# Kernel tuning notes

Hardware: AMD Instinct MI355X
Metric: run time of the kernel (lower is better)

The kernel has to match this reference:

```python
import jax, jax.numpy as jnp
import numpy as np


def setup_inputs() -> dict:
    key = jax.random.key(0)
    pcd = jax.random.normal(key, (8, 4096, 3), dtype=jnp.float32)
    return {"pcd": pcd, "k": 5}


def reference(pcd, k):
    # pcd: [B, N, 3]. Faithful port of MC3DAD_ONNX.get_geometry_features.
    sq = jnp.sum(pcd * pcd, axis=-1)                       # [B, N]
    d2 = sq[:, :, None] + sq[:, None, :] - 2.0 * jnp.einsum('bnd,bmd->bnm', pcd, pcd)
    dist = jnp.sqrt(jnp.maximum(d2, 0.0))                  # [B, N, N], == torch.cdist
    # k nearest neighbors (smallest distances) -> indices only
    _, idx = jax.lax.top_k(-dist, k)                       # idx: [B, N, K]
    # gather neighbor coordinates: [B, N, K, 3]
    neighbors = jax.vmap(lambda p, i: p[i])(pcd, idx)
    centroid = jnp.mean(neighbors, axis=2, keepdims=True)  # [B, N, 1, 3]
    centered = neighbors - centroid                        # [B, N, K, 3]
    # per-point 3x3 covariance: centered^T @ centered / (K-1)
    cov = jnp.einsum('bnkc,bnkd->bncd', centered, centered) / (k - 1)
    trace = jnp.trace(cov, axis1=-2, axis2=-1)             # [B, N]
    curvature = trace / (jnp.sum(trace, axis=-1, keepdims=True) + 1e-8)
    return curvature
```

## Files before the change

kernel.cpp:

```cpp
#include <hip/hip_runtime.h>
#include <hip/hip_bf16.h>


typedef unsigned long long ull;

constexpr int N_PTS  = 4096;
constexpr int BATCH  = 8;
constexpr int KNN    = 5;
constexpr int SEG    = 8;
constexpr int SEGLEN = N_PTS / SEG;
constexpr int QPW    = 8;
constexpr int NTHR   = 1024;
constexpr int QPB    = (NTHR / 64) * QPW;
constexpr int KSLOT  = 16;
constexpr int TRIG   = KSLOT - 4;

__device__ __forceinline__ int swz(int j) { return j + (j >> 9); }

__device__ __forceinline__ ull umin64(ull a, ull b) { return a < b ? a : b; }
__device__ __forceinline__ ull umax64(ull a, ull b) { return a < b ? b : a; }

__device__ __forceinline__ void push5(float dd, int idx,
                                      float d[KNN], int ix[KNN])
{
    float ad = dd; int ai = idx;
    #pragma unroll
    for (int p = 0; p < KNN - 1; ++p) {
        const bool lt = ad < d[p];
        const float md = lt ? ad : d[p];
        const int   mi = lt ? ai : ix[p];
        const float xd = lt ? d[p] : ad;
        const int   xi = lt ? ix[p] : ai;
        d[p] = md; ix[p] = mi; ad = xd; ai = xi;
    }
    const bool lt = ad < d[KNN - 1];
    d[KNN - 1]  = lt ? ad : d[KNN - 1];
    ix[KNN - 1] = lt ? ai : ix[KNN - 1];
}

__device__ __forceinline__ void merge5(ull a[KNN], const ull b[KNN])
{
    const ull r0 = umin64(a[0], b[0]);
    const ull r1 = umin64(umin64(a[1], b[1]), umax64(a[0], b[0]));
    const ull r2 = umin64(umin64(a[2], b[2]),
                          umin64(umax64(a[1], b[0]), umax64(a[0], b[1])));
    const ull r3 = umin64(umin64(a[3], b[3]),
                   umin64(umax64(a[2], b[0]),
                   umin64(umax64(a[1], b[1]), umax64(a[0], b[2]))));
    const ull r4 = umin64(umin64(a[4], b[4]),
                   umin64(umin64(umax64(a[3], b[0]), umax64(a[2], b[1])),
                          umin64(umax64(a[1], b[2]), umax64(a[0], b[3]))));
    a[0] = r0; a[1] = r1; a[2] = r2; a[3] = r3; a[4] = r4;
}

struct KnnShared {
    float4 pts[N_PTS + SEG];
    int    buf[KSLOT * NTHR];
};

__device__ __forceinline__ void drain_buf(int& cnt, const float4 qp,
                                          float dq[KNN], int iq[KNN],
                                          float& tau_q,
                                          const float4* __restrict__ pts,
                                          const int* __restrict__ lanebuf)
{
    for (int j = 0; ; ++j) {
        if (!__any(j < cnt)) break;
        if (j < cnt) {
            const int idx = lanebuf[j * NTHR];
            const float4 c = pts[swz(idx)];
            const float dot = __fadd_rn(__fadd_rn(__fmul_rn(qp.x, c.x),
                                                  __fmul_rn(qp.y, c.y)),
                                        __fmul_rn(qp.z, c.z));
            const float dd = __fsub_rn(__fadd_rn(qp.w, c.w),
                                       __fmul_rn(2.0f, dot));
            push5(dd, idx, dq, iq);
        }
    }
    cnt = 0;
    tau_q = __fsub_rn(dq[KNN - 1], qp.w) + 6e-5f;
}

__global__ __launch_bounds__(NTHR, 4)
void knn_trace_kernel(const float* __restrict__ pcd, float* __restrict__ trace_out)
{
    __shared__ KnnShared sh;

    const int b = blockIdx.y;
    const int t = threadIdx.x;
    const float* __restrict__ batch = pcd + (size_t)b * N_PTS * 3;

    #pragma unroll
    for (int i = 0; i < N_PTS / NTHR; ++i) {
        const int p = t + i * NTHR;
        const float x = batch[p * 3 + 0];
        const float y = batch[p * 3 + 1];
        const float z = batch[p * 3 + 2];
        const float sq = __fadd_rn(__fadd_rn(__fmul_rn(x, x), __fmul_rn(y, y)),
                                   __fmul_rn(z, z));
        sh.pts[swz(p)] = make_float4(x, y, z, sq);
    }
    __syncthreads();

    const int lane = t & 63;
    const int wave = t >> 6;
    const int q    = lane & 7;
    const int s    = lane >> 3;
    const int qbase = blockIdx.x * QPB + wave * QPW;
    const float4 qp = sh.pts[swz(qbase + q)];

    float dq[KNN];
    int   iq[KNN];
    #pragma unroll
    for (int r = 0; r < KNN; ++r) { dq[r] = __builtin_inff(); iq[r] = 0x7fffffff; }

    const float4* __restrict__ seg = sh.pts + (s * SEGLEN + s);
    int* __restrict__ lanebuf = sh.buf + t;

    int   cnt   = 0;
    float tau_q = __builtin_inff();
    const int idx0 = s * SEGLEN;

    for (int m0 = 0; m0 < SEGLEN; m0 += 4) {
        #pragma unroll
        for (int u = 0; u < 4; ++u) {
            const float4 c = seg[m0 + u];
            const float t2 = fmaf(-2.0f,
                                  fmaf(qp.x, c.x,
                                       fmaf(qp.y, c.y, qp.z * c.z)),
                                  c.w);
            const bool keep = t2 < tau_q;
            lanebuf[cnt * NTHR] = idx0 + m0 + u;
            cnt += keep ? 1 : 0;
        }
        if (__any(cnt > TRIG))
            drain_buf(cnt, qp, dq, iq, tau_q, sh.pts, lanebuf);
    }
    drain_buf(cnt, qp, dq, iq, tau_q, sh.pts, lanebuf);

    ull key[KNN];
    #pragma unroll
    for (int r = 0; r < KNN; ++r) {
        const float dist = __fsqrt_rn(fmaxf(dq[r], 0.0f));
        key[r] = ((ull)__float_as_uint(dist) << 32) | (unsigned)iq[r];
    }
    #pragma unroll
    for (int i = 0; i < KNN - 1; ++i)
        #pragma unroll
        for (int p = 0; p < KNN - 1 - i; ++p) {
            const ull lo = umin64(key[p], key[p + 1]);
            const ull hi = umax64(key[p], key[p + 1]);
            key[p] = lo; key[p + 1] = hi;
        }

    #pragma unroll
    for (int mask = 8; mask < 64; mask <<= 1) {
        ull o[KNN];
        #pragma unroll
        for (int r = 0; r < KNN; ++r) o[r] = __shfl_xor(key[r], mask);
        merge5(key, o);
    }

    if (lane < 8) {
        float nx[KNN], ny[KNN], nz[KNN];
        #pragma unroll
        for (int r = 0; r < KNN; ++r) {
            const int sel = (int)(key[r] & 0xffffffffull);
            const float4 p = sh.pts[swz(sel)];
            nx[r] = p.x; ny[r] = p.y; nz[r] = p.z;
        }

        float sx = nx[0], sy = ny[0], sz = nz[0];
        #pragma unroll
        for (int r = 1; r < KNN; ++r) {
            sx = __fadd_rn(sx, nx[r]);
            sy = __fadd_rn(sy, ny[r]);
            sz = __fadd_rn(sz, nz[r]);
        }
        const float cx = __fdiv_rn(sx, 5.0f);
        const float cy = __fdiv_rn(sy, 5.0f);
        const float cz = __fdiv_rn(sz, 5.0f);

        float sxx = 0.0f, syy = 0.0f, szz = 0.0f;
        #pragma unroll
        for (int r = 0; r < KNN; ++r) {
            const float dx = __fsub_rn(nx[r], cx);
            const float dy = __fsub_rn(ny[r], cy);
            const float dz = __fsub_rn(nz[r], cz);
            sxx = __fadd_rn(sxx, __fmul_rn(dx, dx));
            syy = __fadd_rn(syy, __fmul_rn(dy, dy));
            szz = __fadd_rn(szz, __fmul_rn(dz, dz));
        }
        const float trace = __fadd_rn(__fadd_rn(__fmul_rn(sxx, 0.25f),
                                                __fmul_rn(syy, 0.25f)),
                                      __fmul_rn(szz, 0.25f));
        trace_out[(size_t)b * N_PTS + qbase + lane] = trace;
    }
}

__global__ __launch_bounds__(256)
void curvature_kernel(const float* __restrict__ trace, float* __restrict__ out)
{
    __shared__ float red[256];
    const int b = blockIdx.x >> 3;
    const int c = blockIdx.x & 7;
    const int t = threadIdx.x;
    const float* __restrict__ tr = trace + (size_t)b * N_PTS;

    float s = 0.0f;
    #pragma unroll
    for (int i = 0; i < N_PTS / 256; ++i)
        s += tr[t + i * 256];
    red[t] = s;
    __syncthreads();
    #pragma unroll
    for (int o = 128; o > 0; o >>= 1) {
        if (t < o) red[t] += red[t + o];
        __syncthreads();
    }
    const float denom = red[0] + 1e-8f;

    float* __restrict__ ob = out + (size_t)b * N_PTS;
    const int x = c * 512 + t;
    ob[x]       = tr[x]       / denom;
    ob[x + 256] = tr[x + 256] / denom;
}

extern "C" void kernel_launch(void* const* d_in, const int* in_sizes, int n_in,
                              void* d_out, int out_size, void* d_ws, size_t ws_size,
                              hipStream_t stream)
{
    (void)in_sizes; (void)n_in; (void)out_size; (void)ws_size;
    const float* pcd = (const float*)d_in[0];
    float* trace = (float*)d_ws;
    float* out = (float*)d_out;

    dim3 gridA(N_PTS / QPB, BATCH);
    knn_trace_kernel<<<gridA, NTHR, 0, stream>>>(pcd, trace);
    curvature_kernel<<<BATCH * 8, 256, 0, stream>>>(trace, out);
}
```

Measured before the change: 135.8 us.

## Replace LDS candidate buffer with bitmask scan and wave-shared pruning threshold

The per-lane LDS index buffer is replaced by register bitmasks: each chunk is scanned to build a keep-mask, and the mask is then drained with ctz. Each lane now handles two queries, reusing every loaded candidate point, and blocks drop to 512 threads. After each chunk the running 5th-best distance is min-reduced across the 8 segment lanes of a query and used as a shared pruning threshold. Chunk sizes grow from 8 to 32 so pruning can start early. This removes LDS buffer traffic and tightens pruning, at the cost of more shuffles and per-chunk synchronisation points.

```diff
diff --git a/kernel.cpp b/kernel.cpp
--- a/kernel.cpp
+++ b/kernel.cpp
@@ -1,5 +1,4 @@
 #include <hip/hip_runtime.h>
-#include <hip/hip_bf16.h>
 
 
 typedef unsigned long long ull;
@@ -9,11 +8,9 @@
 constexpr int KNN    = 5;
 constexpr int SEG    = 8;
 constexpr int SEGLEN = N_PTS / SEG;
-constexpr int QPW    = 8;
-constexpr int NTHR   = 1024;
+constexpr int NTHR   = 512;
+constexpr int QPW    = 16;
 constexpr int QPB    = (NTHR / 64) * QPW;
-constexpr int KSLOT  = 16;
-constexpr int TRIG   = KSLOT - 4;
 
 __device__ __forceinline__ int swz(int j) { return j + (j >> 9); }
 
@@ -53,38 +50,89 @@
     a[0] = r0; a[1] = r1; a[2] = r2; a[3] = r3; a[4] = r4;
 }
 
-struct KnnShared {
-    float4 pts[N_PTS + SEG];
-    int    buf[KSLOT * NTHR];
-};
-
-__device__ __forceinline__ void drain_buf(int& cnt, const float4 qp,
-                                          float dq[KNN], int iq[KNN],
-                                          float& tau_q,
-                                          const float4* __restrict__ pts,
-                                          const int* __restrict__ lanebuf)
-{
-    for (int j = 0; ; ++j) {
-        if (!__any(j < cnt)) break;
-        if (j < cnt) {
-            const int idx = lanebuf[j * NTHR];
+__device__ __forceinline__ void sort5(ull key[KNN])
+{
+    #pragma unroll
+    for (int i = 0; i < KNN - 1; ++i)
+        #pragma unroll
+        for (int p = 0; p < KNN - 1 - i; ++p) {
+            const ull lo = umin64(key[p], key[p + 1]);
+            const ull hi = umax64(key[p], key[p + 1]);
+            key[p] = lo; key[p + 1] = hi;
+        }
+}
+
+template<int CSZ>
+__device__ __forceinline__ void scan_chunk(const float4* __restrict__ seg, int step0,
+                                           const float4 p0, const float4 p1,
+                                           const float tau0, const float tau1,
+                                           unsigned& m0, unsigned& m1)
+{
+    unsigned a = 0, b = 0;
+    #pragma unroll 8
+    for (int u = 0; u < CSZ; ++u) {
+        const float4 c = seg[step0 + u];
+        const float f0 = fmaf(-2.0f, fmaf(p0.x, c.x,
+                                          fmaf(p0.y, c.y, p0.z * c.z)), c.w);
+        const float f1 = fmaf(-2.0f, fmaf(p1.x, c.x,
+                                          fmaf(p1.y, c.y, p1.z * c.z)), c.w);
+        a = (a << 1) | (f0 < tau0 ? 1u : 0u);
+        b = (b << 1) | (f1 < tau1 ? 1u : 0u);
+    }
+    m0 = a; m1 = b;
+}
+
+__device__ __forceinline__ void drain_pair(unsigned r0, unsigned r1, int base,
+                                           const float4 p0, const float4 p1,
+                                           float* __restrict__ d0, int* __restrict__ i0,
+                                           float* __restrict__ d1, int* __restrict__ i1,
+                                           const float4* __restrict__ pts)
+{
+    while (__any((r0 | r1) != 0)) {
+        if (r0) {
+            const int bpos = __builtin_ctz(r0);
+            r0 &= r0 - 1;
+            const int idx = base + bpos;
             const float4 c = pts[swz(idx)];
-            const float dot = __fadd_rn(__fadd_rn(__fmul_rn(qp.x, c.x),
-                                                  __fmul_rn(qp.y, c.y)),
-                                        __fmul_rn(qp.z, c.z));
-            const float dd = __fsub_rn(__fadd_rn(qp.w, c.w),
+            const float dot = __fadd_rn(__fadd_rn(__fmul_rn(p0.x, c.x),
+                                                  __fmul_rn(p0.y, c.y)),
+                                        __fmul_rn(p0.z, c.z));
+            const float dd = __fsub_rn(__fadd_rn(p0.w, c.w),
                                        __fmul_rn(2.0f, dot));
-            push5(dd, idx, dq, iq);
-        }
-    }
-    cnt = 0;
-    tau_q = __fsub_rn(dq[KNN - 1], qp.w) + 6e-5f;
-}
-
-__global__ __launch_bounds__(NTHR, 4)
+            push5(dd, idx, d0, i0);
+        }
+        if (r1) {
+            const int bpos = __builtin_ctz(r1);
+            r1 &= r1 - 1;
+            const int idx = base + bpos;
+            const float4 c = pts[swz(idx)];
+            const float dot = __fadd_rn(__fadd_rn(__fmul_rn(p1.x, c.x),
+                                                  __fmul_rn(p1.y, c.y)),
+                                        __fmul_rn(p1.z, c.z));
+            const float dd = __fsub_rn(__fadd_rn(p1.w, c.w),
+                                       __fmul_rn(2.0f, dot));
+            push5(dd, idx, d1, i1);
+        }
+    }
+}
+
+__device__ __forceinline__ void share_tau(const float4 p0, const float4 p1,
+                                          float d0_4, float d1_4,
+                                          float& tau0, float& tau1)
+{
+    #pragma unroll
+    for (int mask = 8; mask < 64; mask <<= 1) {
+        d0_4 = fminf(d0_4, __shfl_xor(d0_4, mask));
+        d1_4 = fminf(d1_4, __shfl_xor(d1_4, mask));
+    }
+    tau0 = __fsub_rn(d0_4, p0.w) + 6e-5f;
+    tau1 = __fsub_rn(d1_4, p1.w) + 6e-5f;
+}
+
+__global__ __launch_bounds__(NTHR, 2)
 void knn_trace_kernel(const float* __restrict__ pcd, float* __restrict__ trace_out)
 {
-    __shared__ KnnShared sh;
+    __shared__ float4 spts[N_PTS + SEG];
 
     const int b = blockIdx.y;
     const int t = threadIdx.x;
@@ -98,75 +146,86 @@
         const float z = batch[p * 3 + 2];
         const float sq = __fadd_rn(__fadd_rn(__fmul_rn(x, x), __fmul_rn(y, y)),
                                    __fmul_rn(z, z));
-        sh.pts[swz(p)] = make_float4(x, y, z, sq);
+        spts[swz(p)] = make_float4(x, y, z, sq);
     }
     __syncthreads();
 
     const int lane = t & 63;
     const int wave = t >> 6;
-    const int q    = lane & 7;
+    const int j    = lane & 7;
     const int s    = lane >> 3;
     const int qbase = blockIdx.x * QPB + wave * QPW;
-    const float4 qp = sh.pts[swz(qbase + q)];
-
-    float dq[KNN];
-    int   iq[KNN];
-    #pragma unroll
-    for (int r = 0; r < KNN; ++r) { dq[r] = __builtin_inff(); iq[r] = 0x7fffffff; }
-
-    const float4* __restrict__ seg = sh.pts + (s * SEGLEN + s);
-    int* __restrict__ lanebuf = sh.buf + t;
-
-    int   cnt   = 0;
-    float tau_q = __builtin_inff();
+
+    const float4 p0 = spts[swz(qbase + j)];
+    const float4 p1 = spts[swz(qbase + 8 + j)];
+
+    float d0[KNN], d1[KNN];
+    int   i0[KNN], i1[KNN];
+    #pragma unroll
+    for (int r = 0; r < KNN; ++r) {
+        d0[r] = __builtin_inff(); i0[r] = 0x7fffffff;
+        d1[r] = __builtin_inff(); i1[r] = 0x7fffffff;
+    }
+    float tau0 = __builtin_inff();
+    float tau1 = __builtin_inff();
+
+    const float4* __restrict__ seg = spts + (s * SEGLEN + s);
     const int idx0 = s * SEGLEN;
 
-    for (int m0 = 0; m0 < SEGLEN; m0 += 4) {
-        #pragma unroll
-        for (int u = 0; u < 4; ++u) {
-            const float4 c = seg[m0 + u];
-            const float t2 = fmaf(-2.0f,
-                                  fmaf(qp.x, c.x,
-                                       fmaf(qp.y, c.y, qp.z * c.z)),
-                                  c.w);
-            const bool keep = t2 < tau_q;
-            lanebuf[cnt * NTHR] = idx0 + m0 + u;
-            cnt += keep ? 1 : 0;
-        }
-        if (__any(cnt > TRIG))
-            drain_buf(cnt, qp, dq, iq, tau_q, sh.pts, lanebuf);
-    }
-    drain_buf(cnt, qp, dq, iq, tau_q, sh.pts, lanebuf);
-
-    ull key[KNN];
+    unsigned m0, m1;
+
+    scan_chunk<8>(seg, 0, p0, p1, tau0, tau1, m0, m1);
+    drain_pair(__brev(m0), __brev(m1), idx0 + 0 - 24, p0, p1, d0, i0, d1, i1, spts);
+    share_tau(p0, p1, d0[KNN - 1], d1[KNN - 1], tau0, tau1);
+
+    scan_chunk<8>(seg, 8, p0, p1, tau0, tau1, m0, m1);
+    drain_pair(__brev(m0), __brev(m1), idx0 + 8 - 24, p0, p1, d0, i0, d1, i1, spts);
+    share_tau(p0, p1, d0[KNN - 1], d1[KNN - 1], tau0, tau1);
+
+    scan_chunk<16>(seg, 16, p0, p1, tau0, tau1, m0, m1);
+    drain_pair(__brev(m0), __brev(m1), idx0 + 16 - 16, p0, p1, d0, i0, d1, i1, spts);
+    share_tau(p0, p1, d0[KNN - 1], d1[KNN - 1], tau0, tau1);
+
+    for (int c = 0; c < 15; ++c) {
+        const int s0 = 32 + c * 32;
+        scan_chunk<32>(seg, s0, p0, p1, tau0, tau1, m0, m1);
+        drain_pair(__brev(m0), __brev(m1), idx0 + s0, p0, p1, d0, i0, d1, i1, spts);
+        share_tau(p0, p1, d0[KNN - 1], d1[KNN - 1], tau0, tau1);
+    }
+
+    ull kA[KNN], kB[KNN];
     #pragma unroll
     for (int r = 0; r < KNN; ++r) {
-        const float dist = __fsqrt_rn(fmaxf(dq[r], 0.0f));
-        key[r] = ((ull)__float_as_uint(dist) << 32) | (unsigned)iq[r];
-    }
-    #pragma unroll
-    for (int i = 0; i < KNN - 1; ++i)
-        #pragma unroll
-        for (int p = 0; p < KNN - 1 - i; ++p) {
-            const ull lo = umin64(key[p], key[p + 1]);
-            const ull hi = umax64(key[p], key[p + 1]);
-            key[p] = lo; key[p + 1] = hi;
-        }
+        const float da = __fsqrt_rn(fmaxf(d0[r], 0.0f));
+        kA[r] = ((ull)__float_as_uint(da) << 32) | (unsigned)i0[r];
+        const float db = __fsqrt_rn(fmaxf(d1[r], 0.0f));
+        kB[r] = ((ull)__float_as_uint(db) << 32) | (unsigned)i1[r];
+    }
+    sort5(kA);
+    sort5(kB);
 
     #pragma unroll
     for (int mask = 8; mask < 64; mask <<= 1) {
-        ull o[KNN];
-        #pragma unroll
-        for (int r = 0; r < KNN; ++r) o[r] = __shfl_xor(key[r], mask);
-        merge5(key, o);
-    }
-
-    if (lane < 8) {
+        ull oA[KNN], oB[KNN];
+        #pragma unroll
+        for (int r = 0; r < KNN; ++r) {
+            oA[r] = __shfl_xor(kA[r], mask);
+            oB[r] = __shfl_xor(kB[r], mask);
+        }
+        merge5(kA, oA);
+        merge5(kB, oB);
+    }
+
+    if (lane < 16) {
+        ull k[KNN];
+        #pragma unroll
+        for (int r = 0; r < KNN; ++r) k[r] = (lane < 8) ? kA[r] : kB[r];
+
         float nx[KNN], ny[KNN], nz[KNN];
         #pragma unroll
         for (int r = 0; r < KNN; ++r) {
-            const int sel = (int)(key[r] & 0xffffffffull);
-            const float4 p = sh.pts[swz(sel)];
+            const int sel = (int)(k[r] & 0xffffffffull);
+            const float4 p = spts[swz(sel)];
             nx[r] = p.x; ny[r] = p.y; nz[r] = p.z;
         }
 
```

Result: faster. 116.7 us (-14.1%).

## Register-block 4 queries per lane with bitmask candidate filter and shared threshold

Applied to the files above, without the earlier changes.

Each lane now handles 4 query points over a 128-point segment, 32 segments per query, so every loaded candidate is reused across 4 queries. The shared-memory candidate buffer is replaced by per-chunk 32-bit keep masks that are drained with ctz loops. Each query's pruning threshold is tightened after every chunk using the minimum 5th-best distance across the 32 lanes scanning it. The block drops to 512 threads and the merge tree grows to 5 shuffle stages per query. This cuts the distance FLOPs per candidate and the LDS traffic, in exchange for higher register pressure and more shuffles.

```diff
diff --git a/kernel.cpp b/kernel.cpp
--- a/kernel.cpp
+++ b/kernel.cpp
@@ -1,5 +1,4 @@
 #include <hip/hip_runtime.h>
-#include <hip/hip_bf16.h>
 
 
 typedef unsigned long long ull;
@@ -7,13 +6,12 @@
 constexpr int N_PTS  = 4096;
 constexpr int BATCH  = 8;
 constexpr int KNN    = 5;
-constexpr int SEG    = 8;
-constexpr int SEGLEN = N_PTS / SEG;
-constexpr int QPW    = 8;
-constexpr int NTHR   = 1024;
+constexpr int NQ     = 4;
+constexpr int GSEG   = 32;
+constexpr int SEGLEN = N_PTS / GSEG;
+constexpr int NTHR   = 512;
+constexpr int QPW    = 2 * NQ;
 constexpr int QPB    = (NTHR / 64) * QPW;
-constexpr int KSLOT  = 16;
-constexpr int TRIG   = KSLOT - 4;
 
 __device__ __forceinline__ int swz(int j) { return j + (j >> 9); }
 
@@ -53,38 +51,87 @@
     a[0] = r0; a[1] = r1; a[2] = r2; a[3] = r3; a[4] = r4;
 }
 
-struct KnnShared {
-    float4 pts[N_PTS + SEG];
-    int    buf[KSLOT * NTHR];
-};
-
-__device__ __forceinline__ void drain_buf(int& cnt, const float4 qp,
-                                          float dq[KNN], int iq[KNN],
-                                          float& tau_q,
-                                          const float4* __restrict__ pts,
-                                          const int* __restrict__ lanebuf)
-{
-    for (int j = 0; ; ++j) {
-        if (!__any(j < cnt)) break;
-        if (j < cnt) {
-            const int idx = lanebuf[j * NTHR];
-            const float4 c = pts[swz(idx)];
-            const float dot = __fadd_rn(__fadd_rn(__fmul_rn(qp.x, c.x),
-                                                  __fmul_rn(qp.y, c.y)),
-                                        __fmul_rn(qp.z, c.z));
-            const float dd = __fsub_rn(__fadd_rn(qp.w, c.w),
-                                       __fmul_rn(2.0f, dot));
-            push5(dd, idx, dq, iq);
-        }
-    }
-    cnt = 0;
-    tau_q = __fsub_rn(dq[KNN - 1], qp.w) + 6e-5f;
+__device__ __forceinline__ void sort5(ull key[KNN])
+{
+    #pragma unroll
+    for (int i = 0; i < KNN - 1; ++i)
+        #pragma unroll
+        for (int p = 0; p < KNN - 1 - i; ++p) {
+            const ull lo = umin64(key[p], key[p + 1]);
+            const ull hi = umax64(key[p], key[p + 1]);
+            key[p] = lo; key[p + 1] = hi;
+        }
+}
+
+template<int LEN>
+__device__ __forceinline__ void scan_chunk(const float4* __restrict__ seg, int start,
+                                           const float4 a[NQ], const float tau[NQ],
+                                           unsigned m[NQ])
+{
+    #pragma unroll
+    for (int q = 0; q < NQ; ++q) m[q] = 0u;
+    #pragma unroll
+    for (int g = 0; g < LEN; g += 4) {
+        float4 cb[4];
+        #pragma unroll
+        for (int u = 0; u < 4; ++u) cb[u] = seg[start + g + u];
+        #pragma unroll
+        for (int u = 0; u < 4; ++u) {
+            #pragma unroll
+            for (int q = 0; q < NQ; ++q) {
+                const float f = fmaf(a[q].x, cb[u].x,
+                                fmaf(a[q].y, cb[u].y,
+                                fmaf(a[q].z, cb[u].z, cb[u].w)));
+                m[q] = (m[q] << 1) | (f < tau[q] ? 1u : 0u);
+            }
+        }
+    }
+}
+
+__device__ __forceinline__ void drain4(unsigned r[NQ], int base,
+                                       const float4 p[NQ],
+                                       float d[NQ][KNN], int ix[NQ][KNN],
+                                       const float4* __restrict__ pts)
+{
+    while (__any((r[0] | r[1] | r[2] | r[3]) != 0u)) {
+        #pragma unroll
+        for (int q = 0; q < NQ; ++q) {
+            if (r[q]) {
+                const int bpos = __builtin_ctz(r[q]);
+                r[q] &= r[q] - 1;
+                const int idx = base + bpos;
+                const float4 c = pts[swz(idx)];
+                const float dot = __fadd_rn(__fadd_rn(__fmul_rn(p[q].x, c.x),
+                                                      __fmul_rn(p[q].y, c.y)),
+                                            __fmul_rn(p[q].z, c.z));
+                const float dd = __fsub_rn(__fadd_rn(p[q].w, c.w),
+                                           __fmul_rn(2.0f, dot));
+                push5(dd, idx, d[q], ix[q]);
+            }
+        }
+    }
+}
+
+__device__ __forceinline__ void share_tau4(const float4 p[NQ],
+                                           const float d[NQ][KNN], float tau[NQ])
+{
+    float m5[NQ];
+    #pragma unroll
+    for (int q = 0; q < NQ; ++q) m5[q] = d[q][KNN - 1];
+    #pragma unroll
+    for (int mask = 2; mask < 64; mask <<= 1)
+        #pragma unroll
+        for (int q = 0; q < NQ; ++q)
+            m5[q] = fminf(m5[q], __shfl_xor(m5[q], mask));
+    #pragma unroll
+    for (int q = 0; q < NQ; ++q)
+        tau[q] = __fsub_rn(m5[q], p[q].w) + 6e-5f;
 }
 
 __global__ __launch_bounds__(NTHR, 4)
 void knn_trace_kernel(const float* __restrict__ pcd, float* __restrict__ trace_out)
 {
-    __shared__ KnnShared sh;
+    __shared__ float4 spts[N_PTS + 8];
 
     const int b = blockIdx.y;
     const int t = threadIdx.x;
@@ -98,103 +145,136 @@
         const float z = batch[p * 3 + 2];
         const float sq = __fadd_rn(__fadd_rn(__fmul_rn(x, x), __fmul_rn(y, y)),
                                    __fmul_rn(z, z));
-        sh.pts[swz(p)] = make_float4(x, y, z, sq);
+        spts[swz(p)] = make_float4(x, y, z, sq);
     }
     __syncthreads();
 
     const int lane = t & 63;
     const int wave = t >> 6;
-    const int q    = lane & 7;
-    const int s    = lane >> 3;
-    const int qbase = blockIdx.x * QPB + wave * QPW;
-    const float4 qp = sh.pts[swz(qbase + q)];
-
-    float dq[KNN];
-    int   iq[KNN];
-    #pragma unroll
-    for (int r = 0; r < KNN; ++r) { dq[r] = __builtin_inff(); iq[r] = 0x7fffffff; }
-
-    const float4* __restrict__ seg = sh.pts + (s * SEGLEN + s);
-    int* __restrict__ lanebuf = sh.buf + t;
-
-    int   cnt   = 0;
-    float tau_q = __builtin_inff();
+    const int j    = lane & 1;
+    const int s    = lane >> 1;
+    const int qbase = blockIdx.x * QPB + wave * QPW + j * NQ;
+
+    float4 p[NQ];
+    float4 a[NQ];
+    #pragma unroll
+    for (int q = 0; q < NQ; ++q) {
+        p[q] = spts[swz(qbase + q)];
+        a[q] = make_float4(__fmul_rn(-2.0f, p[q].x),
+                           __fmul_rn(-2.0f, p[q].y),
+                           __fmul_rn(-2.0f, p[q].z), 0.0f);
+    }
+
+    float d[NQ][KNN];
+    int   ix[NQ][KNN];
+    #pragma unroll
+    for (int q = 0; q < NQ; ++q)
+        #pragma unroll
+        for (int r = 0; r < KNN; ++r) { d[q][r] = __builtin_inff(); ix[q][r] = 0x7fffffff; }
+
+    const float4* __restrict__ seg = spts + (s * SEGLEN + (s >> 2));
     const int idx0 = s * SEGLEN;
-
-    for (int m0 = 0; m0 < SEGLEN; m0 += 4) {
-        #pragma unroll
-        for (int u = 0; u < 4; ++u) {
-            const float4 c = seg[m0 + u];
-            const float t2 = fmaf(-2.0f,
-                                  fmaf(qp.x, c.x,
-                                       fmaf(qp.y, c.y, qp.z * c.z)),
-                                  c.w);
-            const bool keep = t2 < tau_q;
-            lanebuf[cnt * NTHR] = idx0 + m0 + u;
-            cnt += keep ? 1 : 0;
-        }
-        if (__any(cnt > TRIG))
-            drain_buf(cnt, qp, dq, iq, tau_q, sh.pts, lanebuf);
-    }
-    drain_buf(cnt, qp, dq, iq, tau_q, sh.pts, lanebuf);
-
-    ull key[KNN];
-    #pragma unroll
-    for (int r = 0; r < KNN; ++r) {
-        const float dist = __fsqrt_rn(fmaxf(dq[r], 0.0f));
-        key[r] = ((ull)__float_as_uint(dist) << 32) | (unsigned)iq[r];
-    }
-    #pragma unroll
-    for (int i = 0; i < KNN - 1; ++i)
-        #pragma unroll
-        for (int p = 0; p < KNN - 1 - i; ++p) {
-            const ull lo = umin64(key[p], key[p + 1]);
-            const ull hi = umax64(key[p], key[p + 1]);
-            key[p] = lo; key[p + 1] = hi;
-        }
-
-    #pragma unroll
-    for (int mask = 8; mask < 64; mask <<= 1) {
-        ull o[KNN];
-        #pragma unroll
-        for (int r = 0; r < KNN; ++r) o[r] = __shfl_xor(key[r], mask);
-        merge5(key, o);
-    }
-
-    if (lane < 8) {
-        float nx[KNN], ny[KNN], nz[KNN];
+    float tau[NQ];
+    unsigned m[NQ], rr[NQ];
+
+    #pragma unroll
+    for (int u = 0; u < 8; ++u) {
+        const float4 c = seg[u];
+        const int idx = idx0 + u;
+        #pragma unroll
+        for (int q = 0; q < NQ; ++q) {
+            const float dot = __fadd_rn(__fadd_rn(__fmul_rn(p[q].x, c.x),
+                                                  __fmul_rn(p[q].y, c.y)),
+                                        __fmul_rn(p[q].z, c.z));
+            const float dd = __fsub_rn(__fadd_rn(p[q].w, c.w),
+                                       __fmul_rn(2.0f, dot));
+            push5(dd, idx, d[q], ix[q]);
+        }
+    }
+    share_tau4(p, d, tau);
+
+    scan_chunk<32>(seg, 8, a, tau, m);
+    #pragma unroll
+    for (int q = 0; q < NQ; ++q) rr[q] = __brev(m[q]);
+    drain4(rr, idx0 + 8, p, d, ix, spts);
+    share_tau4(p, d, tau);
+
+    scan_chunk<32>(seg, 40, a, tau, m);
+    #pragma unroll
+    for (int q = 0; q < NQ; ++q) rr[q] = __brev(m[q]);
+    drain4(rr, idx0 + 40, p, d, ix, spts);
+    share_tau4(p, d, tau);
+
+    scan_chunk<32>(seg, 72, a, tau, m);
+    #pragma unroll
+    for (int q = 0; q < NQ; ++q) rr[q] = __brev(m[q]);
+    drain4(rr, idx0 + 72, p, d, ix, spts);
+    share_tau4(p, d, tau);
+
+    scan_chunk<24>(seg, 104, a, tau, m);
+    #pragma unroll
+    for (int q = 0; q < NQ; ++q) rr[q] = __brev(m[q]);
+    drain4(rr, idx0 + 104 - 8, p, d, ix, spts);
+
+    ull key[NQ][KNN];
+    #pragma unroll
+    for (int q = 0; q < NQ; ++q) {
         #pragma unroll
         for (int r = 0; r < KNN; ++r) {
-            const int sel = (int)(key[r] & 0xffffffffull);
-            const float4 p = sh.pts[swz(sel)];
-            nx[r] = p.x; ny[r] = p.y; nz[r] = p.z;
-        }
-
-        float sx = nx[0], sy = ny[0], sz = nz[0];
-        #pragma unroll
-        for (int r = 1; r < KNN; ++r) {
-            sx = __fadd_rn(sx, nx[r]);
-            sy = __fadd_rn(sy, ny[r]);
-            sz = __fadd_rn(sz, nz[r]);
-        }
-        const float cx = __fdiv_rn(sx, 5.0f);
-        const float cy = __fdiv_rn(sy, 5.0f);
-        const float cz = __fdiv_rn(sz, 5.0f);
-
-        float sxx = 0.0f, syy = 0.0f, szz = 0.0f;
-        #pragma unroll
-        for (int r = 0; r < KNN; ++r) {
-            const float dx = __fsub_rn(nx[r], cx);
-            const float dy = __fsub_rn(ny[r], cy);
-            const float dz = __fsub_rn(nz[r], cz);
-            sxx = __fadd_rn(sxx, __fmul_rn(dx, dx));
-            syy = __fadd_rn(syy, __fmul_rn(dy, dy));
-            szz = __fadd_rn(szz, __fmul_rn(dz, dz));
-        }
-        const float trace = __fadd_rn(__fadd_rn(__fmul_rn(sxx, 0.25f),
-                                                __fmul_rn(syy, 0.25f)),
-                                      __fmul_rn(szz, 0.25f));
-        trace_out[(size_t)b * N_PTS + qbase + lane] = trace;
+            const float dist = __fsqrt_rn(fmaxf(d[q][r], 0.0f));
+            key[q][r] = ((ull)__float_as_uint(dist) << 32) | (unsigned)ix[q][r];
+        }
+        sort5(key[q]);
+    }
+
+    #pragma unroll
+    for (int mask = 2; mask < 64; mask <<= 1) {
+        #pragma unroll
+        for (int q = 0; q < NQ; ++q) {
+            ull o[KNN];
+            #pragma unroll
+            for (int r = 0; r < KNN; ++r) o[r] = __shfl_xor(key[q][r], mask);
+            merge5(key[q], o);
+        }
+    }
+
+    if (lane < 2) {
+        #pragma unroll
+        for (int q = 0; q < NQ; ++q) {
+            float nx[KNN], ny[KNN], nz[KNN];
+            #pragma unroll
+            for (int r = 0; r < KNN; ++r) {
+                const int sel = (int)(key[q][r] & 0xffffffffull);
+                const float4 c = spts[swz(sel)];
+                nx[r] = c.x; ny[r] = c.y; nz[r] = c.z;
+            }
+
+            float sx = nx[0], sy = ny[0], sz = nz[0];
+            #pragma unroll
+            for (int r = 1; r < KNN; ++r) {
+                sx = __fadd_rn(sx, nx[r]);
+                sy = __fadd_rn(sy, ny[r]);
+                sz = __fadd_rn(sz, nz[r]);
+            }
+            const float cx = __fdiv_rn(sx, 5.0f);
+            const float cy = __fdiv_rn(sy, 5.0f);
+            const float cz = __fdiv_rn(sz, 5.0f);
+
+            float sxx = 0.0f, syy = 0.0f, szz = 0.0f;
+            #pragma unroll
+            for (int r = 0; r < KNN; ++r) {
+                const float dx = __fsub_rn(nx[r], cx);
+                const float dy = __fsub_rn(ny[r], cy);
+                const float dz = __fsub_rn(nz[r], cz);
+                sxx = __fadd_rn(sxx, __fmul_rn(dx, dx));
+                syy = __fadd_rn(syy, __fmul_rn(dy, dy));
+                szz = __fadd_rn(szz, __fmul_rn(dz, dz));
+            }
+            const float trace = __fadd_rn(__fadd_rn(__fmul_rn(sxx, 0.25f),
+                                                    __fmul_rn(syy, 0.25f)),
+                                          __fmul_rn(szz, 0.25f));
+            trace_out[(size_t)b * N_PTS + qbase + q] = trace;
+        }
     }
 }
 
```

Measured after the change: 364.0 us. +168.0%, slower.
